# Kernel tuning notes

Hardware: AMD Instinct MI355X
Metric: run time of the kernel (lower is better)

The kernel has to match this reference:

```python
import jax, jax.numpy as jnp
import numpy as np
import math

B, L, M = 8, 1024, 1024
H, D, DK, DFF = 16, 1024, 64, 4096
EPS = 1e-5


def _ln(x, g, b):
    mu = jnp.mean(x, axis=-1, keepdims=True)
    var = jnp.mean((x - mu) ** 2, axis=-1, keepdims=True)
    return (x - mu) * jax.lax.rsqrt(var + EPS) * g + b


def _mha(x, kv, Wq, bq, Wk, bk, Wv, bv, Wo, bo, masked):
    # x: [B,Lq,D], kv: [B,Lk,D]; per-head weights stacked: Wq [H,D,DK], bq [H,DK]
    Q = jnp.einsum('bld,hdk->bhlk', x, Wq) + bq[None, :, None, :]
    K = jnp.einsum('bld,hdk->bhlk', kv, Wk) + bk[None, :, None, :]
    V = jnp.einsum('bld,hdk->bhlk', kv, Wv) + bv[None, :, None, :]
    scores = jnp.einsum('bhqk,bhmk->bhqm', Q, K) / math.sqrt(DK)
    p = jax.nn.softmax(scores, axis=-1)
    if masked:
        # faithful to source: mask applied AFTER softmax (multiply by tril ones)
        Lq = x.shape[1]
        tril = jnp.tril(jnp.ones((Lq, kv.shape[1]), dtype=p.dtype))
        p = p * tril
    z = jnp.einsum('bhqm,bhmk->bhqk', p, V)  # [B,H,Lq,DK]
    z = jnp.transpose(z, (0, 2, 1, 3)).reshape(x.shape[0], x.shape[1], H * DK)
    return z @ Wo + bo


def _forward(x, enc, Wq1, bq1, Wk1, bk1, Wv1, bv1, Wo1, bo1,
             Wq2, bq2, Wk2, bk2, Wv2, bv2, Wo2, bo2,
             W1, b1, W2, b2, g1, be1, g2, be2, g3, be3):
    z = _mha(x, x, Wq1, bq1, Wk1, bk1, Wv1, bv1, Wo1, bo1, masked=True)
    x = _ln(z + x, g1, be1)
    z = _mha(x, enc, Wq2, bq2, Wk2, bk2, Wv2, bv2, Wo2, bo2, masked=False)
    x = _ln(z + x, g2, be2)
    # Conv1d(k=1) pair == per-token MLP: relu(x @ W1 + b1) @ W2 + b2
    y = jax.nn.relu(x @ W1 + b1) @ W2 + b2
    return _ln(y + x, g3, be3)


def setup_inputs() -> dict:
    key = jax.random.key(0)
    ks = jax.random.split(key, 16)
    s = 0.02
    return {
        'x': jax.random.normal(ks[0], (B, L, D), jnp.float32),
        'enc': jax.random.normal(ks[1], (B, M, D), jnp.float32),
        'Wq1': jax.random.normal(ks[2], (H, D, DK), jnp.float32) * s,
        'bq1': jnp.zeros((H, DK), jnp.float32),
        'Wk1': jax.random.normal(ks[3], (H, D, DK), jnp.float32) * s,
        'bk1': jnp.zeros((H, DK), jnp.float32),
        'Wv1': jax.random.normal(ks[4], (H, D, DK), jnp.float32) * s,
        'bv1': jnp.zeros((H, DK), jnp.float32),
        'Wo1': jax.random.normal(ks[5], (H * DK, D), jnp.float32) * s,
        'bo1': jnp.zeros((D,), jnp.float32),
        'Wq2': jax.random.normal(ks[6], (H, D, DK), jnp.float32) * s,
        'bq2': jnp.zeros((H, DK), jnp.float32),
        'Wk2': jax.random.normal(ks[7], (H, D, DK), jnp.float32) * s,
        'bk2': jnp.zeros((H, DK), jnp.float32),
        'Wv2': jax.random.normal(ks[8], (H, D, DK), jnp.float32) * s,
        'bv2': jnp.zeros((H, DK), jnp.float32),
        'Wo2': jax.random.normal(ks[9], (H * DK, D), jnp.float32) * s,
        'bo2': jnp.zeros((D,), jnp.float32),
        'W1': jax.random.normal(ks[10], (D, DFF), jnp.float32) * s,
        'b1': jnp.zeros((DFF,), jnp.float32),
        'W2': jax.random.normal(ks[11], (DFF, D), jnp.float32) * s,
        'b2': jnp.zeros((D,), jnp.float32),
        'g1': jnp.ones((D,), jnp.float32), 'be1': jnp.zeros((D,), jnp.float32),
        'g2': jnp.ones((D,), jnp.float32), 'be2': jnp.zeros((D,), jnp.float32),
        'g3': jnp.ones((D,), jnp.float32), 'be3': jnp.zeros((D,), jnp.float32),
    }


def reference(x, enc, Wq1, bq1, Wk1, bk1, Wv1, bv1, Wo1, bo1,
              Wq2, bq2, Wk2, bk2, Wv2, bv2, Wo2, bo2,
              W1, b1, W2, b2, g1, be1, g2, be2, g3, be3):
    return _forward(x, enc, Wq1, bq1, Wk1, bk1, Wv1, bv1, Wo1, bo1,
                    Wq2, bq2, Wk2, bk2, Wv2, bv2, Wo2, bo2,
                    W1, b1, W2, b2, g1, be1, g2, be2, g3, be3)
```

## Files before the change

### kernel.cpp

```cpp
#include <hip/hip_runtime.h>
#include <hip/hip_bf16.h>

typedef __bf16 bf16;
typedef __bf16 bf16x8 __attribute__((ext_vector_type(8)));
typedef __bf16 bf16x4v __attribute__((ext_vector_type(4)));
typedef float f32x4 __attribute__((ext_vector_type(4)));
typedef unsigned int u32;
typedef u32 u32x4 __attribute__((ext_vector_type(4)));

#define DEV static __device__ __forceinline__

DEV void gll16(const void* g, void* l) {
  __builtin_amdgcn_global_load_lds((__attribute__((address_space(1))) void*)g,
                                   (__attribute__((address_space(3))) void*)l,
                                   16, 0, 0);
}

DEV bf16 tobf(float f) { return (bf16)f; }

DEV u32 cvtpk(float lo, float hi) {
  u32 r;
  asm("v_cvt_pk_bf16_f32 %0, %1, %2" : "=v"(r) : "v"(lo), "v"(hi));
  return r;
}

__global__ void cast_f2b_kernel(const float* __restrict__ in, bf16* __restrict__ out, int n4) {
  int i = blockIdx.x * 256 + threadIdx.x;
  if (i < n4) {
    const float4 v = ((const float4*)in)[i];
    bf16x4v o;
    o[0] = tobf(v.x); o[1] = tobf(v.y); o[2] = tobf(v.z); o[3] = tobf(v.w);
    ((bf16x4v*)out)[i] = o;
  }
}

__global__ __launch_bounds__(256)
void tpack_kernel(const float* __restrict__ in, bf16* __restrict__ out,
                  int K, int N, int in_hs, int out_hs, float scale) {
  __shared__ float tile[32][33];
  const int k0 = blockIdx.x << 5, n0 = blockIdx.y << 5;
  const float* ip = in + (size_t)blockIdx.z * in_hs;
  bf16* op = out + (size_t)blockIdx.z * out_hs;
  const int tx = threadIdx.x & 31, ty = threadIdx.x >> 5;
#pragma unroll
  for (int r = 0; r < 4; ++r)
    tile[ty * 4 + r][tx] = ip[(size_t)(k0 + ty * 4 + r) * N + n0 + tx];
  __syncthreads();
#pragma unroll
  for (int r = 0; r < 4; ++r)
    op[(size_t)(n0 + ty * 4 + r) * K + k0 + tx] = tobf(tile[tx][ty * 4 + r] * scale);
}

__global__ void bscale_kernel(const float* __restrict__ in, float* __restrict__ out, int n, float s) {
  int i = blockIdx.x * 256 + threadIdx.x;
  if (i < n) out[i] = in[i] * s;
}

template<int EPI>
__global__ __launch_bounds__(256, 2)
void gemm_bt(const bf16* __restrict__ A, const bf16* __restrict__ W,
             const float* __restrict__ bias, const float* __restrict__ resid,
             void* __restrict__ outv, int M, int N, int K) {
  __shared__ bf16 sA[2][128 * 64];
  __shared__ bf16 sB[2][128 * 64];
  const int nbx = N >> 7;
  const int nwg = (M >> 7) * nbx;
  int bid = (int)blockIdx.x;
  bid = (bid & 7) * (nwg >> 3) + (bid >> 3);
  const int tm = bid / nbx, tn = bid - tm * nbx;
  const int tid = threadIdx.x;
  const int lane = tid & 63;
  const int w = tid >> 6;
  const int wm = (w >> 1) << 6, wn = (w & 1) << 6;
  const int l15 = lane & 15, l4 = lane >> 4;

  int srow[4], scol[4];
#pragma unroll
  for (int j = 0; j < 4; ++j) {
    int g = tid + (j << 8);
    srow[j] = g >> 3;
    scol[j] = ((g & 7) ^ (srow[j] & 7)) << 3;
  }
  const bf16* Abase = A + (size_t)(tm * 128) * K;
  const bf16* Bbase = W + (size_t)(tn * 128) * K;

  f32x4 acc[4][4] = {};
  const int nt = K >> 6;
  int cur = 0;

  auto stage = [&](int buf, int t) {
    const int kb = t << 6;
#pragma unroll
    for (int j = 0; j < 4; ++j) {
      int g = tid + (j << 8);
      gll16(Abase + (size_t)srow[j] * K + kb + scol[j], &sA[buf][g << 3]);
    }
#pragma unroll
    for (int j = 0; j < 4; ++j) {
      int g = tid + (j << 8);
      gll16(Bbase + (size_t)srow[j] * K + kb + scol[j], &sB[buf][g << 3]);
    }
  };

  stage(0, 0);
  __syncthreads();

  for (int t = 0; t < nt; ++t) {
    if (t + 1 < nt) stage(cur ^ 1, t + 1);
    bf16x8 af[4][2], bfm[4][2];
#pragma unroll
    for (int mi = 0; mi < 4; ++mi)
#pragma unroll
      for (int kk = 0; kk < 2; ++kk) {
        int r = wm + (mi << 4) + l15;
        int off = (r << 7) + (kk << 6) + (l4 << 4);
        off ^= (r & 7) << 4;
        af[mi][kk] = *(const bf16x8*)((const char*)sA[cur] + off);
      }
#pragma unroll
    for (int ni = 0; ni < 4; ++ni)
#pragma unroll
      for (int kk = 0; kk < 2; ++kk) {
        int r = wn + (ni << 4) + l15;
        int off = (r << 7) + (kk << 6) + (l4 << 4);
        off ^= (r & 7) << 4;
        bfm[ni][kk] = *(const bf16x8*)((const char*)sB[cur] + off);
      }
#pragma unroll
    for (int mi = 0; mi < 4; ++mi)
#pragma unroll
      for (int ni = 0; ni < 4; ++ni)
#pragma unroll
        for (int kk = 0; kk < 2; ++kk)
          acc[mi][ni] = __builtin_amdgcn_mfma_f32_16x16x32_bf16(af[mi][kk], bfm[ni][kk],
                                                                acc[mi][ni], 0, 0, 0);
    __syncthreads();
    cur ^= 1;
  }

  const int row0 = tm * 128 + wm + (l4 << 2);
  const int col0 = tn * 128 + wn + l15;
#pragma unroll
  for (int ni = 0; ni < 4; ++ni) {
    const int col = col0 + (ni << 4);
    const float bv = bias ? bias[col] : 0.f;
#pragma unroll
    for (int mi = 0; mi < 4; ++mi) {
      const int rr = row0 + (mi << 4);
      f32x4 v = acc[mi][ni];
      if (EPI == 0) {
        bf16* out = (bf16*)outv;
#pragma unroll
        for (int r = 0; r < 4; ++r) out[(size_t)(rr + r) * N + col] = tobf(v[r] + bv);
      } else if (EPI == 1) {
        float* out = (float*)outv;
#pragma unroll
        for (int r = 0; r < 4; ++r) {
          size_t idx = (size_t)(rr + r) * N + col;
          out[idx] = v[r] + bv + resid[idx];
        }
      } else if (EPI == 2) {
        bf16* out = (bf16*)outv;
#pragma unroll
        for (int r = 0; r < 4; ++r) out[(size_t)(rr + r) * N + col] = tobf(fmaxf(v[r] + bv, 0.f));
      } else if (EPI == 3) {
        bf16* out = (bf16*)outv;
        const int bb = rr >> 10, l0 = rr & 1023;
        const int hh = col >> 6, dk = col & 63;
        bf16x4v pk;
#pragma unroll
        for (int r = 0; r < 4; ++r) pk[r] = tobf(v[r] + bv);
        *(bf16x4v*)(out + ((size_t)((bb * 16 + hh) * 64 + dk) << 10) + l0) = pk;
      } else {
        bf16* out = (bf16*)outv;
        const int seg = tn >> 3;
        const int cc = col & 1023;
        const bool isV = (EPI == 4) ? (seg == 2) : (seg == 1);
        if (isV) {
          bf16* vout = out + (size_t)seg * 8388608;
          const int bb = rr >> 10, l0 = rr & 1023;
          const int hh = cc >> 6, dk = cc & 63;
          bf16x4v pk;
#pragma unroll
          for (int r = 0; r < 4; ++r) pk[r] = tobf(v[r] + bv);
          *(bf16x4v*)(vout + ((size_t)((bb * 16 + hh) * 64 + dk) << 10) + l0) = pk;
        } else {
          bf16* qout = out + (size_t)seg * 8388608;
#pragma unroll
          for (int r = 0; r < 4; ++r) qout[(size_t)(rr + r) * 1024 + cc] = tobf(v[r] + bv);
        }
      }
    }
  }
}

template<bool MASKED>
__global__ __launch_bounds__(256, 3)
void attn_kernel(const bf16* __restrict__ Qp, const bf16* __restrict__ Kp,
                 const bf16* __restrict__ Vt, bf16* __restrict__ Z) {
  __shared__ bf16 sK[2][64 * 64];
  __shared__ bf16 sV[2][64 * 64];
  const int Lk = 1024;
  const int d = blockIdx.x;
  const int bh = d & 127, qb = d >> 7;
  const int b = bh >> 4, h = bh & 15;
  const int q0 = qb << 7;
  const int tid = threadIdx.x, lane = tid & 63, w = tid >> 6;
  const int l15 = lane & 15, l4 = lane >> 4;

  const bf16* Qb = Qp + ((size_t)(b * 1024 + q0 + w * 32)) * 1024 + h * 64;
  bf16x8 qf[2][2];
#pragma unroll
  for (int mi = 0; mi < 2; ++mi)
#pragma unroll
    for (int kk = 0; kk < 2; ++kk)
      qf[mi][kk] = *(const bf16x8*)(Qb + (size_t)((mi << 4) + l15) * 1024 + (kk << 5) + (l4 << 3));

  f32x4 o[4][2] = {};
  float Mr[2] = {-1e30f, -1e30f}, Lr[2] = {0.f, 0.f};

  const bf16* Kb = Kp + ((size_t)b * Lk) * 1024 + h * 64;
  const bf16* Vb = Vt + ((size_t)(b * 16 + h)) * 64 * Lk;

  auto stage = [&](int buf, int t, bool withV) {
    const int kv0 = t << 6;
#pragma unroll
    for (int j = 0; j < 2; ++j) {
      int g = tid + (j << 8);
      int r = g >> 3;
      int sc = ((g & 7) ^ (r & 7)) << 3;
      gll16(Kb + (size_t)(kv0 + r) * 1024 + sc, &sK[buf][g << 3]);
      if (withV) gll16(Vb + (size_t)r * Lk + kv0 + sc, &sV[buf][g << 3]);
    }
  };
  auto needPV = [&](int t) -> bool { return !MASKED || ((t << 6) < q0 + 128); };

  const int NT = Lk >> 6;
  stage(0, 0, true);
  __syncthreads();
  int cur = 0;

  for (int t = 0; t < NT; ++t) {
    if (t + 1 < NT) stage(cur ^ 1, t + 1, needPV(t + 1));
    const int kv0 = t << 6;

    f32x4 s[4][2] = {};
#pragma unroll
    for (int n = 0; n < 4; ++n) {
      bf16x8 kf[2];
#pragma unroll
      for (int kk = 0; kk < 2; ++kk) {
        int r = (n << 4) + l15;
        int off = (r << 7) + (kk << 6) + (l4 << 4);
        off ^= (r & 7) << 4;
        kf[kk] = *(const bf16x8*)((const char*)sK[cur] + off);
      }
#pragma unroll
      for (int mi = 0; mi < 2; ++mi)
#pragma unroll
        for (int kk = 0; kk < 2; ++kk)
          s[n][mi] = __builtin_amdgcn_mfma_f32_16x16x32_bf16(kf[kk], qf[mi][kk],
                                                             s[n][mi], 0, 0, 0);
    }

    float alv[2];
#pragma unroll
    for (int mi = 0; mi < 2; ++mi) {
      float tmx = s[0][mi][0];
#pragma unroll
      for (int n = 0; n < 4; ++n)
#pragma unroll
        for (int r = 0; r < 4; ++r) tmx = fmaxf(tmx, s[n][mi][r]);
      tmx = fmaxf(tmx, __shfl_xor(tmx, 16, 64));
      tmx = fmaxf(tmx, __shfl_xor(tmx, 32, 64));
      const float Mn = fmaxf(Mr[mi], tmx);
      alv[mi] = exp2f(Mr[mi] - Mn);
      float rs = 0.f;
#pragma unroll
      for (int n = 0; n < 4; ++n)
#pragma unroll
        for (int r = 0; r < 4; ++r) {
          float p = exp2f(s[n][mi][r] - Mn);
          s[n][mi][r] = p;
          rs += p;
        }
      rs += __shfl_xor(rs, 16, 64);
      rs += __shfl_xor(rs, 32, 64);
      Lr[mi] = Lr[mi] * alv[mi] + rs;
      Mr[mi] = Mn;
    }

#pragma unroll
    for (int mi = 0; mi < 2; ++mi)
#pragma unroll
      for (int r = 0; r < 4; ++r) {
        float a = __shfl(alv[mi], (l4 << 2) + r, 64);
#pragma unroll
        for (int nd = 0; nd < 4; ++nd) o[nd][mi][r] *= a;
      }

    if (needPV(t)) {
      const bool needMask = MASKED && (kv0 + 63 > q0 + (w << 5));
      bf16x8 pa[2][2];
#pragma unroll
      for (int mi = 0; mi < 2; ++mi) {
        u32 D0[4], D1[4];
        const int qg = q0 + (w << 5) + (mi << 4) + l15;
#pragma unroll
        for (int n = 0; n < 4; ++n) {
          float pv[4];
#pragma unroll
          for (int r = 0; r < 4; ++r) {
            float p = s[n][mi][r];
            if (needMask) {
              int cg = kv0 + (n << 4) + (l4 << 2) + r;
              if (cg > qg) p = 0.f;
            }
            pv[r] = p;
          }
          D0[n] = cvtpk(pv[0], pv[1]);
          D1[n] = cvtpk(pv[2], pv[3]);
        }
        const int src = l15 + ((lane & 16) << 1);
#pragma unroll
        for (int kk = 0; kk < 2; ++kk) {
          u32 v0 = (lane & 32) ? D0[2 * kk + 1] : D0[2 * kk];
          u32 v1 = (lane & 32) ? D1[2 * kk + 1] : D1[2 * kk];
          u32x4 tw;
          tw[0] = (u32)__shfl((int)v0, src, 64);
          tw[1] = (u32)__shfl((int)v1, src, 64);
          tw[2] = (u32)__shfl((int)v0, src + 16, 64);
          tw[3] = (u32)__shfl((int)v1, src + 16, 64);
          pa[mi][kk] = *(bf16x8*)&tw;
        }
      }
#pragma unroll
      for (int nd = 0; nd < 4; ++nd) {
        bf16x8 vf[2];
#pragma unroll
        for (int kk = 0; kk < 2; ++kk) {
          int r = (nd << 4) + l15;
          int off = (r << 7) + (kk << 6) + (l4 << 4);
          off ^= (r & 7) << 4;
          vf[kk] = *(const bf16x8*)((const char*)sV[cur] + off);
        }
#pragma unroll
        for (int mi = 0; mi < 2; ++mi)
#pragma unroll
          for (int kk = 0; kk < 2; ++kk)
            o[nd][mi] = __builtin_amdgcn_mfma_f32_16x16x32_bf16(pa[mi][kk], vf[kk],
                                                                o[nd][mi], 0, 0, 0);
      }
    }
    __syncthreads();
    cur ^= 1;
  }

  float inv[2][4];
#pragma unroll
  for (int mi = 0; mi < 2; ++mi) {
    float il = 1.f / Lr[mi];
#pragma unroll
    for (int r = 0; r < 4; ++r) inv[mi][r] = __shfl(il, (l4 << 2) + r, 64);
  }
  bf16* Zb = Z + ((size_t)(b * 1024 + q0 + w * 32)) * 1024 + h * 64;
#pragma unroll
  for (int nd = 0; nd < 4; ++nd)
#pragma unroll
    for (int mi = 0; mi < 2; ++mi)
#pragma unroll
      for (int r = 0; r < 4; ++r)
        Zb[(size_t)((mi << 4) + (l4 << 2) + r) * 1024 + (nd << 4) + l15] =
            tobf(o[nd][mi][r] * inv[mi][r]);
}

__global__ __launch_bounds__(256)
void ln_kernel(const float* __restrict__ in, const float* __restrict__ gw,
               const float* __restrict__ bw, float* __restrict__ outf,
               bf16* __restrict__ outb) {
  const int row = blockIdx.x, tid = threadIdx.x;
  const size_t base = (size_t)row << 10;
  const float4 v = *(const float4*)(in + base + tid * 4);
  float s = v.x + v.y + v.z + v.w;
  float ss = v.x * v.x + v.y * v.y + v.z * v.z + v.w * v.w;
#pragma unroll
  for (int d = 1; d < 64; d <<= 1) { s += __shfl_xor(s, d, 64); ss += __shfl_xor(ss, d, 64); }
  __shared__ float red[8];
  const int w = tid >> 6;
  if ((tid & 63) == 0) { red[w] = s; red[4 + w] = ss; }
  __syncthreads();
  s = red[0] + red[1] + red[2] + red[3];
  ss = red[4] + red[5] + red[6] + red[7];
  const float mu = s * (1.f / 1024.f);
  const float var = ss * (1.f / 1024.f) - mu * mu;
  const float rstd = rsqrtf(var + 1e-5f);
  const float4 g4 = *(const float4*)(gw + tid * 4);
  const float4 b4 = *(const float4*)(bw + tid * 4);
  const float o0 = (v.x - mu) * rstd * g4.x + b4.x;
  const float o1 = (v.y - mu) * rstd * g4.y + b4.y;
  const float o2 = (v.z - mu) * rstd * g4.z + b4.z;
  const float o3 = (v.w - mu) * rstd * g4.w + b4.w;
  if (outf) { float4 of; of.x = o0; of.y = o1; of.z = o2; of.w = o3;
              *(float4*)(outf + base + tid * 4) = of; }
  if (outb) { bf16x4v ob; ob[0] = tobf(o0); ob[1] = tobf(o1); ob[2] = tobf(o2); ob[3] = tobf(o3);
              *(bf16x4v*)(outb + base + tid * 4) = ob; }
}

extern "C" void kernel_launch(void* const* d_in, const int* in_sizes, int n_in,
                              void* d_out, int out_size, void* d_ws, size_t ws_size,
                              hipStream_t stream) {
  const float* x   = (const float*)d_in[0];
  const float* enc = (const float*)d_in[1];
  const float* Wq1 = (const float*)d_in[2];
  const float* bq1 = (const float*)d_in[3];
  const float* Wk1 = (const float*)d_in[4];
  const float* bk1 = (const float*)d_in[5];
  const float* Wv1 = (const float*)d_in[6];
  const float* bv1 = (const float*)d_in[7];
  const float* Wo1 = (const float*)d_in[8];
  const float* bo1 = (const float*)d_in[9];
  const float* Wq2 = (const float*)d_in[10];
  const float* bq2 = (const float*)d_in[11];
  const float* Wk2 = (const float*)d_in[12];
  const float* bk2 = (const float*)d_in[13];
  const float* Wv2 = (const float*)d_in[14];
  const float* bv2 = (const float*)d_in[15];
  const float* Wo2 = (const float*)d_in[16];
  const float* bo2 = (const float*)d_in[17];
  const float* W1  = (const float*)d_in[18];
  const float* b1  = (const float*)d_in[19];
  const float* W2  = (const float*)d_in[20];
  const float* b2  = (const float*)d_in[21];
  const float* g1  = (const float*)d_in[22];
  const float* be1 = (const float*)d_in[23];
  const float* g2  = (const float*)d_in[24];
  const float* be2 = (const float*)d_in[25];
  const float* g3  = (const float*)d_in[26];
  const float* be3 = (const float*)d_in[27];

  char* ws = (char*)d_ws;
  size_t off = 0;
  auto alloc = [&](size_t bytes) { char* p = ws + off; off += (bytes + 255) & ~(size_t)255; return p; };
  const size_t ACT = (size_t)8 * 1024 * 1024 * 2;
  const float QSC = 0.125f * 1.44269504088896f;

  bf16* xb     = (bf16*)alloc(ACT);
  bf16* encb   = (bf16*)alloc(ACT);
  bf16* Wqkv1t = (bf16*)alloc((size_t)3072 * 1024 * 2);
  bf16* Wkv2t  = (bf16*)alloc((size_t)2048 * 1024 * 2);
  bf16* Wq2t   = (bf16*)alloc((size_t)1024 * 1024 * 2);
  bf16* Wo1t   = (bf16*)alloc((size_t)1024 * 1024 * 2);
  bf16* Wo2t   = (bf16*)alloc((size_t)1024 * 1024 * 2);
  bf16* W1t    = (bf16*)alloc((size_t)4096 * 1024 * 2);
  bf16* W2t    = (bf16*)alloc((size_t)4096 * 1024 * 2);
  float* qkvb1 = (float*)alloc(3072 * 4);
  float* kvb2  = (float*)alloc(2048 * 4);
  float* sbq2  = (float*)alloc(1024 * 4);
  char*  S     = alloc((size_t)64 * 1024 * 1024);
  float* rbuf  = (float*)alloc((size_t)8 * 1024 * 1024 * 4);
  float* xnf   = (float*)alloc((size_t)8 * 1024 * 1024 * 4);
  bf16*  xnb   = (bf16*)alloc(ACT);

  bf16* q1   = (bf16*)(S);
  bf16* k1   = (bf16*)(S + ACT);
  bf16* vt1  = (bf16*)(S + 2 * ACT);
  bf16* z1   = (bf16*)(S + 3 * ACT);
  bf16* hbuf = (bf16*)S;

  dim3 b256(256);
  cast_f2b_kernel<<<8192, b256, 0, stream>>>(x, xb, 2097152);
  cast_f2b_kernel<<<8192, b256, 0, stream>>>(enc, encb, 2097152);
  tpack_kernel<<<dim3(32, 2, 16), b256, 0, stream>>>(Wq1, Wqkv1t, 1024, 64, 65536, 65536, QSC);
  tpack_kernel<<<dim3(32, 2, 16), b256, 0, stream>>>(Wk1, Wqkv1t + 1048576, 1024, 64, 65536, 65536, 1.f);
  tpack_kernel<<<dim3(32, 2, 16), b256, 0, stream>>>(Wv1, Wqkv1t + 2097152, 1024, 64, 65536, 65536, 1.f);
  tpack_kernel<<<dim3(32, 2, 16), b256, 0, stream>>>(Wq2, Wq2t, 1024, 64, 65536, 65536, QSC);
  tpack_kernel<<<dim3(32, 2, 16), b256, 0, stream>>>(Wk2, Wkv2t, 1024, 64, 65536, 65536, 1.f);
  tpack_kernel<<<dim3(32, 2, 16), b256, 0, stream>>>(Wv2, Wkv2t + 1048576, 1024, 64, 65536, 65536, 1.f);
  tpack_kernel<<<dim3(32, 32, 1), b256, 0, stream>>>(Wo1, Wo1t, 1024, 1024, 0, 0, 1.f);
  tpack_kernel<<<dim3(32, 32, 1), b256, 0, stream>>>(Wo2, Wo2t, 1024, 1024, 0, 0, 1.f);
  tpack_kernel<<<dim3(32, 128, 1), b256, 0, stream>>>(W1, W1t, 1024, 4096, 0, 0, 1.f);
  tpack_kernel<<<dim3(128, 32, 1), b256, 0, stream>>>(W2, W2t, 4096, 1024, 0, 0, 1.f);
  bscale_kernel<<<4, b256, 0, stream>>>(bq1, qkvb1, 1024, QSC);
  bscale_kernel<<<4, b256, 0, stream>>>(bk1, qkvb1 + 1024, 1024, 1.f);
  bscale_kernel<<<4, b256, 0, stream>>>(bv1, qkvb1 + 2048, 1024, 1.f);
  bscale_kernel<<<4, b256, 0, stream>>>(bk2, kvb2, 1024, 1.f);
  bscale_kernel<<<4, b256, 0, stream>>>(bv2, kvb2 + 1024, 1024, 1.f);
  bscale_kernel<<<4, b256, 0, stream>>>(bq2, sbq2, 1024, QSC);

  gemm_bt<4><<<1536, b256, 0, stream>>>(xb, Wqkv1t, qkvb1, nullptr, q1, 8192, 3072, 1024);
  attn_kernel<true><<<1024, b256, 0, stream>>>(q1, k1, vt1, z1);
  gemm_bt<1><<<512, b256, 0, stream>>>(z1, Wo1t, bo1, x, rbuf, 8192, 1024, 1024);
  ln_kernel<<<8192, b256, 0, stream>>>(rbuf, g1, be1, xnf, xnb);

  gemm_bt<0><<<512, b256, 0, stream>>>(xnb, Wq2t, sbq2, nullptr, q1, 8192, 1024, 1024);
  gemm_bt<5><<<1024, b256, 0, stream>>>(encb, Wkv2t, kvb2, nullptr, k1, 8192, 2048, 1024);
  attn_kernel<false><<<1024, b256, 0, stream>>>(q1, k1, vt1, z1);
  gemm_bt<1><<<512, b256, 0, stream>>>(z1, Wo2t, bo2, xnf, rbuf, 8192, 1024, 1024);
  ln_kernel<<<8192, b256, 0, stream>>>(rbuf, g2, be2, xnf, xnb);

  gemm_bt<2><<<2048, b256, 0, stream>>>(xnb, W1t, b1, nullptr, hbuf, 8192, 4096, 1024);
  gemm_bt<1><<<512, b256, 0, stream>>>(hbuf, W2t, b2, xnf, rbuf, 8192, 1024, 4096);
  ln_kernel<<<8192, b256, 0, stream>>>(rbuf, g3, be3, (float*)d_out, nullptr);
}
```

Baseline: 645.3 us.

## Replace GEMM with 256x128 8-wave triple-buffered ping-pong pipelined kernel

Result: no change. 633.2 us (-1.9%).

```diff
diff --git a/kernel.cpp b/kernel.cpp
--- a/kernel.cpp
+++ b/kernel.cpp
@@ -57,89 +57,126 @@
 }
 
 template<int EPI>
-__global__ __launch_bounds__(256, 2)
-void gemm_bt(const bf16* __restrict__ A, const bf16* __restrict__ W,
-             const float* __restrict__ bias, const float* __restrict__ resid,
-             void* __restrict__ outv, int M, int N, int K) {
-  __shared__ bf16 sA[2][128 * 64];
-  __shared__ bf16 sB[2][128 * 64];
+__global__ __launch_bounds__(512, 2)
+void gemm8(const bf16* __restrict__ A, const bf16* __restrict__ W,
+           const float* __restrict__ bias, const float* __restrict__ resid,
+           void* __restrict__ outv, int M, int N, int K) {
+  __shared__ bf16 sA[3][256 * 64];
+  __shared__ bf16 sB[3][128 * 64];
   const int nbx = N >> 7;
-  const int nwg = (M >> 7) * nbx;
+  const int nwg = (M >> 8) * nbx;
   int bid = (int)blockIdx.x;
   bid = (bid & 7) * (nwg >> 3) + (bid >> 3);
   const int tm = bid / nbx, tn = bid - tm * nbx;
   const int tid = threadIdx.x;
   const int lane = tid & 63;
   const int w = tid >> 6;
-  const int wm = (w >> 1) << 6, wn = (w & 1) << 6;
+  const int wr = w >> 1, wc = w & 1;
   const int l15 = lane & 15, l4 = lane >> 4;
 
-  int srow[4], scol[4];
-#pragma unroll
-  for (int j = 0; j < 4; ++j) {
-    int g = tid + (j << 8);
-    srow[j] = g >> 3;
-    scol[j] = ((g & 7) ^ (srow[j] & 7)) << 3;
-  }
-  const bf16* Abase = A + (size_t)(tm * 128) * K;
+  const bf16* Abase = A + (size_t)(tm * 256) * K;
   const bf16* Bbase = W + (size_t)(tn * 128) * K;
 
   f32x4 acc[4][4] = {};
   const int nt = K >> 6;
-  int cur = 0;
-
-  auto stage = [&](int buf, int t) {
-    const int kb = t << 6;
+
+  auto stageA = [&](int buf, int t) {
 #pragma unroll
     for (int j = 0; j < 4; ++j) {
-      int g = tid + (j << 8);
-      gll16(Abase + (size_t)srow[j] * K + kb + scol[j], &sA[buf][g << 3]);
-    }
-#pragma unroll
-    for (int j = 0; j < 4; ++j) {
-      int g = tid + (j << 8);
-      gll16(Bbase + (size_t)srow[j] * K + kb + scol[j], &sB[buf][g << 3]);
+      int g = tid + (j << 9);
+      int row = g >> 3;
+      int sc = ((g & 7) ^ (row & 7)) << 3;
+      gll16(Abase + (size_t)row * K + (t << 6) + sc, &sA[buf][g << 3]);
     }
   };
-
-  stage(0, 0);
-  __syncthreads();
-
+  auto stageB = [&](int buf, int t) {
+#pragma unroll
+    for (int j = 0; j < 2; ++j) {
+      int g = tid + (j << 9);
+      int row = g >> 3;
+      int sc = ((g & 7) ^ (row & 7)) << 3;
+      gll16(Bbase + (size_t)row * K + (t << 6) + sc, &sB[buf][g << 3]);
+    }
+  };
+
+  stageA(0, 0); stageB(0, 0);
+  stageA(1, 1 < nt ? 1 : 0); stageB(1, 1 < nt ? 1 : 0);
+  __builtin_amdgcn_sched_barrier(0);
+  asm volatile("s_waitcnt vmcnt(6)" ::: "memory");
+  __builtin_amdgcn_s_barrier();
+
+  int c = 0;
   for (int t = 0; t < nt; ++t) {
-    if (t + 1 < nt) stage(cur ^ 1, t + 1);
-    bf16x8 af[4][2], bfm[4][2];
+    const int sb = (c >= 1) ? c - 1 : 2;
+    const int ts = (t + 2 < nt) ? t + 2 : nt - 1;
+    bf16x8 af[4][2], bfr[4][2];
 #pragma unroll
     for (int mi = 0; mi < 4; ++mi)
 #pragma unroll
       for (int kk = 0; kk < 2; ++kk) {
-        int r = wm + (mi << 4) + l15;
+        int r = wr * 64 + (mi << 4) + l15;
         int off = (r << 7) + (kk << 6) + (l4 << 4);
         off ^= (r & 7) << 4;
-        af[mi][kk] = *(const bf16x8*)((const char*)sA[cur] + off);
-      }
-#pragma unroll
-    for (int ni = 0; ni < 4; ++ni)
+        af[mi][kk] = *(const bf16x8*)((const char*)sA[c] + off);
+      }
+#pragma unroll
+    for (int ni = 0; ni < 2; ++ni)
 #pragma unroll
       for (int kk = 0; kk < 2; ++kk) {
-        int r = wn + (ni << 4) + l15;
+        int r = wc * 64 + (ni << 4) + l15;
         int off = (r << 7) + (kk << 6) + (l4 << 4);
         off ^= (r & 7) << 4;
-        bfm[ni][kk] = *(const bf16x8*)((const char*)sB[cur] + off);
-      }
+        bfr[ni][kk] = *(const bf16x8*)((const char*)sB[c] + off);
+      }
+    stageA(sb, ts);
+    __builtin_amdgcn_sched_barrier(0);
+    __builtin_amdgcn_s_barrier();
+    asm volatile("s_waitcnt lgkmcnt(0)" ::: "memory");
+    __builtin_amdgcn_sched_barrier(0);
+    __builtin_amdgcn_s_setprio(1);
 #pragma unroll
     for (int mi = 0; mi < 4; ++mi)
 #pragma unroll
-      for (int ni = 0; ni < 4; ++ni)
+      for (int ni = 0; ni < 2; ++ni)
 #pragma unroll
         for (int kk = 0; kk < 2; ++kk)
-          acc[mi][ni] = __builtin_amdgcn_mfma_f32_16x16x32_bf16(af[mi][kk], bfm[ni][kk],
+          acc[mi][ni] = __builtin_amdgcn_mfma_f32_16x16x32_bf16(af[mi][kk], bfr[ni][kk],
                                                                 acc[mi][ni], 0, 0, 0);
-    __syncthreads();
-    cur ^= 1;
+    __builtin_amdgcn_s_setprio(0);
+    __builtin_amdgcn_sched_barrier(0);
+    __builtin_amdgcn_s_barrier();
+#pragma unroll
+    for (int ni = 2; ni < 4; ++ni)
+#pragma unroll
+      for (int kk = 0; kk < 2; ++kk) {
+        int r = wc * 64 + (ni << 4) + l15;
+        int off = (r << 7) + (kk << 6) + (l4 << 4);
+        off ^= (r & 7) << 4;
+        bfr[ni][kk] = *(const bf16x8*)((const char*)sB[c] + off);
+      }
+    stageB(sb, ts);
+    __builtin_amdgcn_sched_barrier(0);
+    asm volatile("s_waitcnt vmcnt(6)" ::: "memory");
+    __builtin_amdgcn_s_barrier();
+    asm volatile("s_waitcnt lgkmcnt(0)" ::: "memory");
+    __builtin_amdgcn_sched_barrier(0);
+    __builtin_amdgcn_s_setprio(1);
+#pragma unroll
+    for (int mi = 0; mi < 4; ++mi)
+#pragma unroll
+      for (int ni = 2; ni < 4; ++ni)
+#pragma unroll
+        for (int kk = 0; kk < 2; ++kk)
+          acc[mi][ni] = __builtin_amdgcn_mfma_f32_16x16x32_bf16(af[mi][kk], bfr[ni][kk],
+                                                                acc[mi][ni], 0, 0, 0);
+    __builtin_amdgcn_s_setprio(0);
+    __builtin_amdgcn_sched_barrier(0);
+    __builtin_amdgcn_s_barrier();
+    c = (c == 2) ? 0 : c + 1;
   }
 
-  const int row0 = tm * 128 + wm + (l4 << 2);
-  const int col0 = tn * 128 + wn + l15;
+  const int row0 = tm * 256 + wr * 64 + (l4 << 2);
+  const int col0 = tn * 128 + wc * 64 + l15;
 #pragma unroll
   for (int ni = 0; ni < 4; ++ni) {
     const int col = col0 + (ni << 4);
@@ -173,7 +210,7 @@
         *(bf16x4v*)(out + ((size_t)((bb * 16 + hh) * 64 + dk) << 10) + l0) = pk;
       } else {
         bf16* out = (bf16*)outv;
-        const int seg = tn >> 3;
+        const int seg = col >> 10;
         const int cc = col & 1023;
         const bool isV = (EPI == 4) ? (seg == 2) : (seg == 1);
         if (isV) {
@@ -195,7 +232,7 @@
 }
 
 template<bool MASKED>
-__global__ __launch_bounds__(256, 3)
+__global__ __launch_bounds__(256, 2)
 void attn_kernel(const bf16* __restrict__ Qp, const bf16* __restrict__ Kp,
                  const bf16* __restrict__ Vt, bf16* __restrict__ Z) {
   __shared__ bf16 sK[2][64 * 64];
@@ -468,6 +505,7 @@
   bf16* hbuf = (bf16*)S;
 
   dim3 b256(256);
+  dim3 b512(512);
   cast_f2b_kernel<<<8192, b256, 0, stream>>>(x, xb, 2097152);
   cast_f2b_kernel<<<8192, b256, 0, stream>>>(enc, encb, 2097152);
   tpack_kernel<<<dim3(32, 2, 16), b256, 0, stream>>>(Wq1, Wqkv1t, 1024, 64, 65536, 65536, QSC);
@@ -487,18 +525,18 @@
   bscale_kernel<<<4, b256, 0, stream>>>(bv2, kvb2 + 1024, 1024, 1.f);
   bscale_kernel<<<4, b256, 0, stream>>>(bq2, sbq2, 1024, QSC);
 
-  gemm_bt<4><<<1536, b256, 0, stream>>>(xb, Wqkv1t, qkvb1, nullptr, q1, 8192, 3072, 1024);
+  gemm8<4><<<768, b512, 0, stream>>>(xb, Wqkv1t, qkvb1, nullptr, q1, 8192, 3072, 1024);
   attn_kernel<true><<<1024, b256, 0, stream>>>(q1, k1, vt1, z1);
-  gemm_bt<1><<<512, b256, 0, stream>>>(z1, Wo1t, bo1, x, rbuf, 8192, 1024, 1024);
+  gemm8<1><<<256, b512, 0, stream>>>(z1, Wo1t, bo1, x, rbuf, 8192, 1024, 1024);
   ln_kernel<<<8192, b256, 0, stream>>>(rbuf, g1, be1, xnf, xnb);
 
-  gemm_bt<0><<<512, b256, 0, stream>>>(xnb, Wq2t, sbq2, nullptr, q1, 8192, 1024, 1024);
-  gemm_bt<5><<<1024, b256, 0, stream>>>(encb, Wkv2t, kvb2, nullptr, k1, 8192, 2048, 1024);
+  gemm8<0><<<256, b512, 0, stream>>>(xnb, Wq2t, sbq2, nullptr, q1, 8192, 1024, 1024);
+  gemm8<5><<<512, b512, 0, stream>>>(encb, Wkv2t, kvb2, nullptr, k1, 8192, 2048, 1024);
   attn_kernel<false><<<1024, b256, 0, stream>>>(q1, k1, vt1, z1);
-  gemm_bt<1><<<512, b256, 0, stream>>>(z1, Wo2t, bo2, xnf, rbuf, 8192, 1024, 1024);
+  gemm8<1><<<256, b512, 0, stream>>>(z1, Wo2t, bo2, xnf, rbuf, 8192, 1024, 1024);
   ln_kernel<<<8192, b256, 0, stream>>>(rbuf, g2, be2, xnf, xnb);
 
-  gemm_bt<2><<<2048, b256, 0, stream>>>(xnb, W1t, b1, nullptr, hbuf, 8192, 4096, 1024);
-  gemm_bt<1><<<512, b256, 0, stream>>>(hbuf, W2t, b2, xnf, rbuf, 8192, 1024, 4096);
+  gemm8<2><<<1024, b512, 0, stream>>>(xnb, W1t, b1, nullptr, hbuf, 8192, 4096, 1024);
+  gemm8<1><<<256, b512, 0, stream>>>(hbuf, W2t, b2, xnf, rbuf, 8192, 1024, 4096);
   ln_kernel<<<8192, b256, 0, stream>>>(rbuf, g3, be3, (float*)d_out, nullptr);
 }
```
